# Kernel optimization log

Measured on AMD Instinct MI355X. Metric: run time of the kernel, lower is better.

The kernel has to match this reference:

```python
import math
import jax, jax.numpy as jnp
import numpy as np
from jax import lax

CELL = 8
BINS = 9


def setup_inputs() -> dict:
    key = jax.random.key(0)
    x = jax.random.uniform(key, (64, 3, 224, 224), dtype=jnp.float32)
    return {"x": x}


def reference(x):
    N, C, H, W = x.shape
    # Fixed Sobel buffers: one output channel summing over all input channels.
    sob = jnp.array([[-1.0, 0.0, 1.0], [-2.0, 0.0, 2.0], [-1.0, 0.0, 1.0]], dtype=x.dtype)
    kx = jnp.broadcast_to(sob, (1, C, 3, 3))          # SobelX weight [O=1, I=C, 3, 3]
    ky = jnp.broadcast_to(sob.T, (1, C, 3, 3))        # SobelY weight
    dn = ('NCHW', 'OIHW', 'NCHW')
    gx = lax.conv_general_dilated(x, kx, (1, 1), 'SAME', dimension_numbers=dn)  # [N,1,H,W]
    gy = lax.conv_general_dilated(x, ky, (1, 1), 'SAME', dimension_numbers=dn)
    mag = jnp.sqrt(gx * gx + gy * gy)                 # [N,1,H,W]
    ang = jnp.abs(jnp.arctan2(gx, gy))                # unsigned gradients -> [0, pi]
    bin_idx = jnp.floor(ang / math.pi * (BINS - 1)).astype(jnp.int32)  # [N,1,H,W], values in [0, BINS-1]
    # scatter_(1, bin_idx, mag) == one-hot along bin axis times magnitude
    onehot = (bin_idx == jnp.arange(BINS, dtype=jnp.int32)[None, :, None, None]).astype(x.dtype)  # [N,BINS,H,W]
    vol = onehot * mag                                # broadcast over bin axis
    # AvgPool2d(cell) * cell^2 == per-cell sum
    hog = vol.reshape(N, BINS, H // CELL, CELL, W // CELL, CELL).sum(axis=(3, 5))  # [N,BINS,H/8,W/8]
    return hog.reshape(N, -1)
```

## Files before the change

### kernel.cpp

```cpp
#include <hip/hip_runtime.h>
#include <math.h>


namespace {
constexpr int Himg = 224;
constexpr int Wimg = 224;
constexpr int NCELL = 28;
constexpr int BINS  = 9;
constexpr int ROWS  = 10;
constexpr int LDSW  = 232;

__global__ __launch_bounds__(256) void hog_kernel(const float* __restrict__ x,
                                                  float* __restrict__ out) {
    const int n  = blockIdx.y;
    const int cr = blockIdx.x;
    const int t  = threadIdx.x;

    __shared__ float s[ROWS][LDSW];
    __shared__ float hist[NCELL * BINS];

    if (t < NCELL * BINS) hist[t] = 0.0f;
    if (t < ROWS * 8) {
        int r = t >> 3;
        int c = t & 7;
        int col = (c < 4) ? c : (224 + c);
        s[r][col] = 0.0f;
    }

    const int h0 = cr * 8 - 1;
    const float* xb = x + (size_t)n * 3 * Himg * Wimg;

    for (int idx = t; idx < ROWS * 56; idx += 256) {
        int r = idx / 56;
        int q = idx - r * 56;
        int w = q * 4;
        int h = h0 + r;
        float4 v = make_float4(0.f, 0.f, 0.f, 0.f);
        if (h >= 0 && h < Himg) {
            const float* r0 = xb + (size_t)h * Wimg;
            const float* r1 = r0 + Himg * Wimg;
            const float* r2 = r1 + Himg * Wimg;
            float4 a = *(const float4*)(r0 + w);
            float4 b = *(const float4*)(r1 + w);
            float4 c4 = *(const float4*)(r2 + w);
            v.x = a.x + b.x + c4.x;
            v.y = a.y + b.y + c4.y;
            v.z = a.z + b.z + c4.z;
            v.w = a.w + b.w + c4.w;
        }
        *(float4*)&s[r][4 + w] = v;
    }
    __syncthreads();

    const int row  = t >> 5;
    const int col0 = t & 31;
    const float PI_F = 3.14159265358979323846f;
    const float CK[8] = {0.92387953f, 0.70710678f, 0.38268343f, 0.0f,
                         -0.38268343f, -0.70710678f, -0.92387953f, -1.0f};

#pragma unroll
    for (int k = 0; k < 7; ++k) {
        int w = col0 + 32 * k;
        const float* sr0 = &s[row][4 + w];
        const float* sr1 = &s[row + 1][4 + w];
        const float* sr2 = &s[row + 2][4 + w];
        float gx = (sr0[1] - sr0[-1]) + 2.0f * (sr1[1] - sr1[-1]) + (sr2[1] - sr2[-1]);
        float gy = (sr2[-1] + 2.0f * sr2[0] + sr2[1]) - (sr0[-1] + 2.0f * sr0[0] + sr0[1]);
        float mag = sqrtf(gx * gx + gy * gy);

        float negy = -gy;
        int bin = 0;
        float guard = 1e30f;
#pragma unroll
        for (int j = 0; j < 8; ++j) {
            float sj = fmaf(mag, CK[j], negy);
            bin += (sj >= 0.0f) ? 1 : 0;
            guard = fminf(guard, fabsf(sj));
        }
        if (guard < mag * 1e-4f) {
            float ang = fabsf(atan2f(gx, gy));
            bin = (int)(ang / PI_F * 8.0f);
            bin = bin > 8 ? 8 : bin;
        }
        atomicAdd(&hist[(w >> 3) * BINS + bin], mag);
    }
    __syncthreads();

    if (t < NCELL * BINS) {
        int bin = t / NCELL;
        int cw  = t - bin * NCELL;
        out[((size_t)n * BINS + bin) * (NCELL * NCELL) + (size_t)cr * NCELL + cw] =
            hist[cw * BINS + bin];
    }
}
}

extern "C" void kernel_launch(void* const* d_in, const int* in_sizes, int n_in,
                              void* d_out, int out_size, void* d_ws, size_t ws_size,
                              hipStream_t stream) {
    const float* x = (const float*)d_in[0];
    float* out = (float*)d_out;
    const int N = in_sizes[0] / (3 * Himg * Wimg);
    dim3 grid(NCELL, N);
    hog_kernel<<<grid, 256, 0, stream>>>(x, out);
}
```

Baseline: 94.07 us.

## Replace LDS atomics with per-column register histograms and sliding Sobel window

Each of 224 threads now walks one column down the 8 cell rows. It keeps a rolling 3-row window in registers and accumulates a 9-bin histogram in registers instead of doing LDS atomicAdd per pixel. Per-column histograms go to LDS, then a final pass reduces 8 columns per cell. This removes atomic contention and redundant LDS reads, but it leaves 32 of the 256 threads idle, lengthens the serial chain per thread, and uses more LDS for the column histograms.

```diff
diff --git a/kernel.cpp b/kernel.cpp
--- a/kernel.cpp
+++ b/kernel.cpp
@@ -17,9 +17,8 @@
     const int t  = threadIdx.x;
 
     __shared__ float s[ROWS][LDSW];
-    __shared__ float hist[NCELL * BINS];
+    __shared__ float h2[Wimg * BINS];
 
-    if (t < NCELL * BINS) hist[t] = 0.0f;
     if (t < ROWS * 8) {
         int r = t >> 3;
         int c = t & 7;
@@ -52,45 +51,60 @@
     }
     __syncthreads();
 
-    const int row  = t >> 5;
-    const int col0 = t & 31;
     const float PI_F = 3.14159265358979323846f;
     const float CK[8] = {0.92387953f, 0.70710678f, 0.38268343f, 0.0f,
                          -0.38268343f, -0.70710678f, -0.92387953f, -1.0f};
 
+    if (t < Wimg) {
+        const int w = t;
+        float ml = s[0][3 + w], mc = s[0][4 + w], mr = s[0][5 + w];
+        float zl = s[1][3 + w], zc = s[1][4 + w], zr = s[1][5 + w];
+        float acc[BINS];
 #pragma unroll
-    for (int k = 0; k < 7; ++k) {
-        int w = col0 + 32 * k;
-        const float* sr0 = &s[row][4 + w];
-        const float* sr1 = &s[row + 1][4 + w];
-        const float* sr2 = &s[row + 2][4 + w];
-        float gx = (sr0[1] - sr0[-1]) + 2.0f * (sr1[1] - sr1[-1]) + (sr2[1] - sr2[-1]);
-        float gy = (sr2[-1] + 2.0f * sr2[0] + sr2[1]) - (sr0[-1] + 2.0f * sr0[0] + sr0[1]);
-        float mag = sqrtf(gx * gx + gy * gy);
+        for (int j = 0; j < BINS; ++j) acc[j] = 0.0f;
 
-        float negy = -gy;
-        int bin = 0;
-        float guard = 1e30f;
 #pragma unroll
-        for (int j = 0; j < 8; ++j) {
-            float sj = fmaf(mag, CK[j], negy);
-            bin += (sj >= 0.0f) ? 1 : 0;
-            guard = fminf(guard, fabsf(sj));
+        for (int i = 0; i < 8; ++i) {
+            float pl = s[i + 2][3 + w];
+            float pc = s[i + 2][4 + w];
+            float pr = s[i + 2][5 + w];
+
+            float gx = (mr - ml) + 2.0f * (zr - zl) + (pr - pl);
+            float gy = (pl + 2.0f * pc + pr) - (ml + 2.0f * mc + mr);
+            float mag = sqrtf(gx * gx + gy * gy);
+
+            float negy = -gy;
+            int bin = 0;
+            float guard = 1e30f;
+#pragma unroll
+            for (int j = 0; j < 8; ++j) {
+                float sj = fmaf(mag, CK[j], negy);
+                bin += (sj >= 0.0f) ? 1 : 0;
+                guard = fminf(guard, fabsf(sj));
+            }
+            if (guard < mag * 1e-4f) {
+                float ang = fabsf(atan2f(gx, gy));
+                bin = (int)(ang / PI_F * 8.0f);
+                bin = bin > 8 ? 8 : bin;
+            }
+#pragma unroll
+            for (int j = 0; j < BINS; ++j) acc[j] += (bin == j) ? mag : 0.0f;
+
+            ml = zl; mc = zc; mr = zr;
+            zl = pl; zc = pc; zr = pr;
         }
-        if (guard < mag * 1e-4f) {
-            float ang = fabsf(atan2f(gx, gy));
-            bin = (int)(ang / PI_F * 8.0f);
-            bin = bin > 8 ? 8 : bin;
-        }
-        atomicAdd(&hist[(w >> 3) * BINS + bin], mag);
+#pragma unroll
+        for (int j = 0; j < BINS; ++j) h2[w * BINS + j] = acc[j];
     }
     __syncthreads();
 
     if (t < NCELL * BINS) {
         int bin = t / NCELL;
         int cw  = t - bin * NCELL;
-        out[((size_t)n * BINS + bin) * (NCELL * NCELL) + (size_t)cr * NCELL + cw] =
-            hist[cw * BINS + bin];
+        float v = 0.0f;
+#pragma unroll
+        for (int c = 0; c < 8; ++c) v += h2[(cw * 8 + c) * BINS + bin];
+        out[((size_t)n * BINS + bin) * (NCELL * NCELL) + (size_t)cr * NCELL + cw] = v;
     }
 }
 }
```

Result: faster. 83.83 us (-10.9%).
